# Optimization experiments

Measured on AMD Instinct MI355X. Metric: run time of the kernel, lower is better.

The kernel has to match this reference:

```python
import jax, jax.numpy as jnp
import numpy as np

N = 131072       # total nodes (B graphs x P nodes)
P = 4096         # nodes per graph
B = 32           # graphs in batch
E = 2097152      # edges (avg degree 16)
IN_DIM = 64
HID = 128
OUT = 16
EPS = 1e-5
SLOPE = 0.01


def _degrees(idx):
    # structural degree, clamped to min 1 (as DGL GraphConv does)
    d = jax.ops.segment_sum(jnp.ones((E,), jnp.float32), idx, num_segments=N)
    return jnp.maximum(d, 1.0)


def _graph_conv(x, W, src, dst, ew):
    # DGL GraphConv, norm='both', bias=False, with scalar edge weights:
    # h = D_out^{-1/2} x ; m_v = sum_{(u->v)} w_e h_u ; out = (D_in^{-1/2} m) W
    h = x * jax.lax.rsqrt(_degrees(src))[:, None]
    m = jax.ops.segment_sum(ew[:, None] * h[src], dst, num_segments=N)  # [N, F]
    return (m * jax.lax.rsqrt(_degrees(dst))[:, None]) @ W


def _graph_norm(x, gamma, beta, alpha):
    # GraphNorm (Cai et al. / PyG, batch=None): stats over all nodes per feature
    mu = jnp.mean(x, axis=0)
    c = x - alpha * mu
    var = jnp.mean(c * c, axis=0)
    return c * jax.lax.rsqrt(var + EPS) * gamma + beta


def _mean_nodes(h, gid):
    # per-graph mean readout; every graph has exactly P nodes
    return jax.ops.segment_sum(h, gid, num_segments=B) / P


def setup_inputs() -> dict:
    key = jax.random.key(0)
    ks = jax.random.split(key, 8)
    src = jax.random.randint(ks[0], (E,), 0, N, dtype=jnp.int32)
    # keep edges within each 4096-node graph block (batched DGL graph)
    dst = (src // P) * P + jax.random.randint(ks[1], (E,), 0, P, dtype=jnp.int32)
    features = jax.random.normal(ks[2], (N, IN_DIM), jnp.float32)
    edge_weights = jax.random.uniform(ks[3], (E,), jnp.float32)
    # kaiming/xavier-scale init approximations
    W1 = jax.random.normal(ks[4], (IN_DIM, HID), jnp.float32) * np.sqrt(2.0 / IN_DIM)
    W2 = jax.random.normal(ks[5], (HID, HID), jnp.float32) * np.sqrt(2.0 / HID)
    Wc = jax.random.normal(ks[6], (OUT, 2 * HID), jnp.float32) * np.sqrt(1.0 / (2 * HID))
    ones = jnp.ones((HID,), jnp.float32)
    zeros = jnp.zeros((HID,), jnp.float32)
    return {
        'features': features, 'edge_weights': edge_weights, 'src': src, 'dst': dst,
        'W1': W1, 'W2': W2, 'Wc': Wc,
        'gamma1': ones, 'beta1': zeros, 'alpha1': ones,
        'gamma2': ones, 'beta2': zeros, 'alpha2': ones,
    }


def reference(features, edge_weights, src, dst, W1, W2, Wc,
              gamma1, beta1, alpha1, gamma2, beta2, alpha2):
    gid = jnp.arange(N, dtype=jnp.int32) // P  # node -> graph id
    h1 = _graph_conv(features, W1, src, dst, edge_weights)
    h1 = jax.nn.leaky_relu(_graph_norm(h1, gamma1, beta1, alpha1), SLOPE)
    r1 = _mean_nodes(h1, gid)                  # [B, HID]
    h2 = _graph_conv(h1, W2, src, dst, edge_weights)
    h2 = jax.nn.leaky_relu(_graph_norm(h2, gamma2, beta2, alpha2), SLOPE)
    r2 = _mean_nodes(h2, gid)                  # [B, HID]
    readouts = jnp.concatenate([r1, r2], axis=1)  # [B, 2*HID]
    return readouts @ Wc.T                     # [B, OUT]
```

## Files before the change

kernel.cpp:

```cpp
#include <hip/hip_runtime.h>
#include <hip/hip_fp16.h>

constexpr int NN   = 131072;
constexpr int PP   = 4096;
constexpr int BG   = 32;
constexpr int EE   = 2097152;
constexpr int IND  = 64;
constexpr int HH   = 128;
constexpr int CAP  = 81920;
constexpr float EPSV   = 1e-5f;
constexpr float SLOPEV = 0.01f;

typedef short bf16x8 __attribute__((ext_vector_type(8)));
typedef float f32x4  __attribute__((ext_vector_type(4)));
typedef float f32x2  __attribute__((ext_vector_type(2)));
typedef unsigned u32x4 __attribute__((ext_vector_type(4)));

__device__ __forceinline__ unsigned f2bf(float f) {
    unsigned u = __float_as_uint(f);
    return (u + 0x7FFFu + ((u >> 16) & 1u)) >> 16;
}
__device__ __forceinline__ unsigned pack2bf(float lo, float hi) {
    return f2bf(lo) | (f2bf(hi) << 16);
}
__device__ __forceinline__ float bflo(unsigned p) { return __uint_as_float(p << 16); }
__device__ __forceinline__ float bfhi(unsigned p) { return __uint_as_float(p & 0xFFFF0000u); }
__device__ __forceinline__ float w16(unsigned r) {
    return __half2float(__ushort_as_half((unsigned short)(r >> 16)));
}

template <int K>
__device__ __forceinline__ void packw_body(const float* __restrict__ W,
                                           unsigned short* __restrict__ pw, int t) {
    if (t >= K * 16) return;
    int lane = t & 63, nt = (t >> 6) & 7, kt = t >> 9;
    int kbase = kt * 32 + ((lane >> 4) & 3) * 8;
    int col   = nt * 16 + (lane & 15);
    for (int j = 0; j < 8; j++)
        pw[t * 8 + j] = (unsigned short)f2bf(W[(kbase + j) * HH + col]);
}

__global__ __launch_bounds__(256) void k_prep(const float* __restrict__ features,
                                              unsigned* __restrict__ f8x,
                                              const float* __restrict__ W1,
                                              unsigned short* __restrict__ pw1,
                                              const float* __restrict__ W2,
                                              unsigned short* __restrict__ pw2,
                                              int* __restrict__ gcur,
                                              float* __restrict__ racc,
                                              unsigned* __restrict__ csr2) {
    int b = blockIdx.x, t = threadIdx.x;
    if (b < 8192) {
        int i = b * 256 + t;
        float4 v = ((const float4*)features)[i];
        int w0 = __builtin_amdgcn_cvt_pk_fp8_f32(v.x, v.y, 0, false);
        int w1 = __builtin_amdgcn_cvt_pk_fp8_f32(v.z, v.w, w0, true);
        f8x[i] = (unsigned)w1;
        return;
    }
    if (b == 8192) {
        if (t < BG) gcur[t * 16] = t * CAP;
        for (int i = t; i < 2 * BG * HH; i += 256) racc[i] = 0.f;
        return;
    }
    if (b < 8197) { packw_body<64>(W1, pw1, (b - 8193) * 256 + t); return; }
    if (b < 8205) { packw_body<128>(W2, pw2, (b - 8197) * 256 + t); return; }
    ((uint4*)csr2)[(b - 8205) * 256 + t] = make_uint4(0, 0, 0, 0);
}

__global__ __launch_bounds__(256) void k_part(const int* __restrict__ src,
                                              const int* __restrict__ dst,
                                              const float* __restrict__ ew,
                                              int* __restrict__ gcur,
                                              uint2* __restrict__ recs) {
    __shared__ int cnt[32];
    __shared__ int start[32];
    __shared__ int gbase[32];
    __shared__ uint2 stage[4096];
    int t = threadIdx.x;
    int ebase = blockIdx.x * 4096;
    if (t < 32) cnt[t] = 0;
    __syncthreads();
    int es[16]; int ed[16]; float ev[16];
#pragma unroll
    for (int k = 0; k < 16; k++) {
        int e = ebase + k * 256 + t;
        es[k] = src[e]; ed[k] = dst[e]; ev[k] = ew[e];
        atomicAdd(&cnt[es[k] >> 12], 1);
    }
    __syncthreads();
    if (t == 0) {
        int run = 0;
        for (int g = 0; g < 32; g++) { start[g] = run; run += cnt[g]; }
    }
    __syncthreads();
    if (t < 32) {
        gbase[t] = atomicAdd(&gcur[t * 16], cnt[t]);
        cnt[t] = start[t];
    }
    __syncthreads();
#pragma unroll
    for (int k = 0; k < 16; k++) {
        int g = es[k] >> 12;
        int pos = atomicAdd(&cnt[g], 1);
        stage[pos] = make_uint2((unsigned)(es[k] & 4095) | ((unsigned)(ed[k] & 4095) << 12) |
                                ((unsigned)g << 24), __float_as_uint(ev[k]));
    }
    __syncthreads();
    for (int i = t; i < 4096; i += 256) {
        uint2 r = stage[i];
        int g = r.x >> 24;
        recs[gbase[g] + (i - start[g])] = r;
    }
}

__global__ __launch_bounds__(1024) void k_hist(const uint2* __restrict__ recs,
                                               const int* __restrict__ gcur,
                                               int* __restrict__ shist,
                                               int* __restrict__ dhist) {
    __shared__ int hs[4096];
    __shared__ int hd[4096];
    int t = threadIdx.x;
    int g = blockIdx.x >> 3, c = blockIdx.x & 7;
    int n = gcur[g * 16] - g * CAP;
    int lo = (n * c) >> 3, hi = (n * (c + 1)) >> 3;
    ((int4*)hs)[t] = make_int4(0, 0, 0, 0);
    ((int4*)hd)[t] = make_int4(0, 0, 0, 0);
    __syncthreads();
    const uint2* base = recs + (size_t)g * CAP;
    for (int i = lo + t; i < hi; i += 1024) {
        unsigned x = base[i].x;
        atomicAdd(&hs[x & 4095], 1);
        atomicAdd(&hd[(x >> 12) & 4095], 1);
    }
    __syncthreads();
    ((int4*)(shist + (size_t)blockIdx.x * 4096))[t] = ((int4*)hs)[t];
    ((int4*)(dhist + (size_t)blockIdx.x * 4096))[t] = ((int4*)hd)[t];
}

__global__ __launch_bounds__(1024) void k_offs(int* __restrict__ shist,
                                               int* __restrict__ dhist,
                                               float* __restrict__ rs_s,
                                               float* __restrict__ rsd,
                                               int* __restrict__ degd,
                                               int* __restrict__ offs) {
    __shared__ int partial[1024];
    int t = threadIdx.x, g = blockIdx.x;
    int sdeg[4] = {0, 0, 0, 0}, ddeg[4] = {0, 0, 0, 0};
#pragma unroll
    for (int c = 0; c < 8; c++) {
        int4 sv = ((const int4*)(shist + (size_t)(g * 8 + c) * 4096))[t];
        int4 dv = ((const int4*)(dhist + (size_t)(g * 8 + c) * 4096))[t];
        sdeg[0] += sv.x; sdeg[1] += sv.y; sdeg[2] += sv.z; sdeg[3] += sv.w;
        ddeg[0] += dv.x; ddeg[1] += dv.y; ddeg[2] += dv.z; ddeg[3] += dv.w;
    }
    int pdeg[4];
#pragma unroll
    for (int j = 0; j < 4; j++) {
        int idx = t * 4 + j;
        int vs = sdeg[j]; if (vs < 1) vs = 1;
        rs_s[g * PP + idx] = rsqrtf((float)vs);
        int vd = ddeg[j]; if (vd < 1) vd = 1;
        rsd[g * PP + idx]  = rsqrtf((float)vd);
        pdeg[j] = (ddeg[j] + 3) & ~3;
        degd[g * PP + idx] = pdeg[j];
    }
    partial[t] = pdeg[0] + pdeg[1] + pdeg[2] + pdeg[3];
    __syncthreads();
    for (int off = 1; off < 1024; off <<= 1) {
        int v = partial[t];
        int add = (t >= off) ? partial[t - off] : 0;
        __syncthreads();
        partial[t] = v + add;
        __syncthreads();
    }
    int run = (t == 0) ? 0 : partial[t - 1];
#pragma unroll
    for (int j = 0; j < 4; j++) {
        int idx = t * 4 + j;
        offs[g * PP + idx] = g * CAP + run;
        int nb = run;
        for (int c = 0; c < 8; c++) {
            size_t hidx = (size_t)(g * 8 + c) * 4096 + idx;
            int v = dhist[hidx];
            dhist[hidx] = nb;
            nb += v;
        }
        run += pdeg[j];
    }
}

__global__ __launch_bounds__(1024) void k_place(const uint2* __restrict__ recs,
                                                const int* __restrict__ gcur,
                                                const int* __restrict__ dhist,
                                                const float* __restrict__ rs_s,
                                                unsigned* __restrict__ csr2) {
    __shared__ int cur[4096];
    __shared__ float rss[4096];
    int t = threadIdx.x;
    int g = blockIdx.x >> 3, c = blockIdx.x & 7;
    int n = gcur[g * 16] - g * CAP;
    int lo = (n * c) >> 3, hi = (n * (c + 1)) >> 3;
    ((int4*)cur)[t] = ((const int4*)(dhist + (size_t)blockIdx.x * 4096))[t];
    ((float4*)rss)[t] = ((const float4*)(rs_s + (size_t)g * PP))[t];
    __syncthreads();
    const uint2* base = recs + (size_t)g * CAP;
    unsigned* cbase = csr2 + (size_t)g * CAP;
    for (int i = lo + t; i < hi; i += 1024) {
        uint2 r = base[i];
        int sl = r.x & 4095, dl = (r.x >> 12) & 4095;
        int pos = atomicAdd(&cur[dl], 1);
        float wf = __uint_as_float(r.y) * rss[sl];
        cbase[pos] = (unsigned)sl | ((unsigned)__half_as_ushort(__float2half(wf)) << 16);
    }
}

__device__ __forceinline__ void eacc8(unsigned rec, unsigned q, f32x2& P01, f32x2& P23) {
    f32x2 lo = __builtin_amdgcn_cvt_pk_f32_fp8((int)q, false);
    f32x2 hi = __builtin_amdgcn_cvt_pk_f32_fp8((int)q, true);
    float w = w16(rec);
    P01 += lo * w;
    P23 += hi * w;
}

template <int ROWW>
__device__ __forceinline__ void gath8(const unsigned* __restrict__ hp, u32x4 r,
                                      unsigned& d0, unsigned& d1, unsigned& d2, unsigned& d3) {
    d0 = hp[(r[0] & 4095u) * ROWW];
    d1 = hp[(r[1] & 4095u) * ROWW];
    d2 = hp[(r[2] & 4095u) * ROWW];
    d3 = hp[(r[3] & 4095u) * ROWW];
}

__device__ __forceinline__ void macc8(u32x4 r, unsigned q0, unsigned q1, unsigned q2, unsigned q3,
                                      f32x2& P01, f32x2& P23) {
    eacc8(r[0], q0, P01, P23); eacc8(r[1], q1, P01, P23);
    eacc8(r[2], q2, P01, P23); eacc8(r[3], q3, P01, P23);
}

template <int ROWW>
__device__ __forceinline__ void agg_dual8(const unsigned* __restrict__ hp,
                                          const u32x4* __restrict__ cs4,
                                          int oa, int ca, int ob, int cb,
                                          f32x2& A01, f32x2& A23, f32x2& B01, f32x2& B23) {
    f32x2 z = {0.f, 0.f};
    A01 = z; A23 = z; B01 = z; B23 = z;
    unsigned a4 = ((unsigned)oa) >> 2, b4 = ((unsigned)ob) >> 2;
    int c0 = ca < cb ? ca : cb;
    int cm = ca < cb ? cb : ca;
    int nq = c0 >> 2;
    if (nq > 0) {
        u32x4 ra0 = __builtin_nontemporal_load(cs4 + a4);
        u32x4 rb0 = __builtin_nontemporal_load(cs4 + b4);
        u32x4 ra1 = __builtin_nontemporal_load(cs4 + a4 + 1);
        u32x4 rb1 = __builtin_nontemporal_load(cs4 + b4 + 1);
        unsigned A0, A1, A2, A3, B0, B1, B2, B3;
        unsigned C0, C1, C2, C3, D0, D1, D2, D3;
        gath8<ROWW>(hp, ra0, A0, A1, A2, A3);
        gath8<ROWW>(hp, rb0, B0, B1, B2, B3);
        int k = 0;
        for (; k + 2 <= nq; k += 2) {
            gath8<ROWW>(hp, ra1, C0, C1, C2, C3);
            gath8<ROWW>(hp, rb1, D0, D1, D2, D3);
            u32x4 ra2 = __builtin_nontemporal_load(cs4 + a4 + k + 2);
            u32x4 rb2 = __builtin_nontemporal_load(cs4 + b4 + k + 2);
            macc8(ra0, A0, A1, A2, A3, A01, A23);
            macc8(rb0, B0, B1, B2, B3, B01, B23);
            gath8<ROWW>(hp, ra2, A0, A1, A2, A3);
            gath8<ROWW>(hp, rb2, B0, B1, B2, B3);
            u32x4 ra3 = __builtin_nontemporal_load(cs4 + a4 + k + 3);
            u32x4 rb3 = __builtin_nontemporal_load(cs4 + b4 + k + 3);
            macc8(ra1, C0, C1, C2, C3, A01, A23);
            macc8(rb1, D0, D1, D2, D3, B01, B23);
            ra0 = ra2; rb0 = rb2; ra1 = ra3; rb1 = rb3;
        }
        if (k < nq) {
            macc8(ra0, A0, A1, A2, A3, A01, A23);
            macc8(rb0, B0, B1, B2, B3, B01, B23);
        }
    }
    if (cm > c0) {
        bool an = ca > cb;
        unsigned t4 = an ? a4 : b4;
        int kq1 = cm >> 2, nq0 = c0 >> 2;
        f32x2 E01 = z, E23 = z;
        u32x4 rr = __builtin_nontemporal_load(cs4 + t4 + nq0);
        for (int k = nq0; k < kq1; k++) {
            unsigned q0, q1, q2, q3;
            gath8<ROWW>(hp, rr, q0, q1, q2, q3);
            u32x4 nr = __builtin_nontemporal_load(cs4 + t4 + k + 1);
            macc8(rr, q0, q1, q2, q3, E01, E23);
            rr = nr;
        }
        if (an) { A01 += E01; A23 += E23; }
        else    { B01 += E01; B23 += E23; }
    }
}

__global__ __launch_bounds__(256) void k_aggemm1(const unsigned* __restrict__ f8x,
                                                 const unsigned* __restrict__ csr2,
                                                 const int* __restrict__ offs,
                                                 const int* __restrict__ degd,
                                                 const float* __restrict__ rsd,
                                                 const short* __restrict__ PW,
                                                 unsigned short* __restrict__ C,
                                                 float* __restrict__ part) {
    constexpr int WP = 36;
    __shared__ unsigned lds[64 * WP];
    __shared__ float s1[HH], s2[HH];
    int t = threadIdx.x;
    if (t < HH) { s1[t] = 0.f; s2[t] = 0.f; }
    int bid = blockIdx.x;
    int xcd = bid & 7, idx = bid >> 3;
    int g = xcd * 4 + (idx >> 6);
    int node0 = g * PP + (idx & 63) * 64;
    int lane = t & 63, wv = t >> 6;
    int q = lane >> 4, ql = lane & 15;
    const unsigned* hp8 = f8x + (size_t)((unsigned)(g * PP)) * 16 + ql;
    const u32x4* cs4 = (const u32x4*)csr2;
#pragma unroll
    for (int p = 0; p < 2; p++) {
        int lrA = wv * 16 + p * 8 + q * 2;
        int va = node0 + lrA;
        int2 oo = *(const int2*)(offs + va);
        int2 dd = *(const int2*)(degd + va);
        f32x2 A01, A23, B01, B23;
        agg_dual8<16>(hp8, cs4, oo.x, dd.x, oo.y, dd.y, A01, A23, B01, B23);
        float2 rr2 = *(const float2*)(rsd + va);
        *(uint2*)&lds[lrA * WP + ql * 2] =
            make_uint2(pack2bf(A01.x * rr2.x, A01.y * rr2.x),
                       pack2bf(A23.x * rr2.x, A23.y * rr2.x));
        *(uint2*)&lds[(lrA + 1) * WP + ql * 2] =
            make_uint2(pack2bf(B01.x * rr2.y, B01.y * rr2.y),
                       pack2bf(B23.x * rr2.y, B23.y * rr2.y));
    }
    __syncthreads();
    int m = lane & 15, quad = lane >> 4;
    bf16x8 a[2];
#pragma unroll
    for (int kt = 0; kt < 2; kt++)
        a[kt] = *(const bf16x8*)&lds[(wv * 16 + m) * WP + kt * 16 + quad * 4];
#pragma unroll
    for (int nt = 0; nt < 8; nt++) {
        f32x4 acc = {0.f, 0.f, 0.f, 0.f};
#pragma unroll
        for (int kt = 0; kt < 2; kt++) {
            bf16x8 b = *(const bf16x8*)(PW + ((size_t)(kt * 8 + nt) * 64 + lane) * 8);
            acc = __builtin_amdgcn_mfma_f32_16x16x32_bf16(a[kt], b, acc, 0, 0, 0);
        }
        int col = nt * 16 + m;
        int r0 = node0 + wv * 16 + quad * 4;
        float ps = 0.f, pq = 0.f;
#pragma unroll
        for (int r = 0; r < 4; r++) {
            C[(size_t)(r0 + r) * HH + col] = (unsigned short)f2bf(acc[r]);
            ps += acc[r]; pq += acc[r] * acc[r];
        }
        atomicAdd(&s1[col], ps);
        atomicAdd(&s2[col], pq);
    }
    __syncthreads();
    if (t < HH) {
        part[bid * 256 + t]      = s1[t];
        part[bid * 256 + HH + t] = s2[t];
    }
}

__global__ __launch_bounds__(256) void k_aggemm2(const unsigned* __restrict__ f8,
                                                 const unsigned* __restrict__ csr2,
                                                 const int* __restrict__ offs,
                                                 const int* __restrict__ degd,
                                                 const float* __restrict__ rsd,
                                                 const short* __restrict__ PW,
                                                 unsigned short* __restrict__ C,
                                                 float* __restrict__ part) {
    constexpr int WP = 68;
    __shared__ unsigned lds[64 * WP];
    __shared__ float s1[HH], s2[HH];
    int t = threadIdx.x;
    if (t < HH) { s1[t] = 0.f; s2[t] = 0.f; }
    int bid = blockIdx.x;
    int xcd = bid & 7, idx = bid >> 3;
    int g = xcd * 4 + (idx >> 6);
    int node0 = g * PP + (idx & 63) * 64;
    int lane = t & 63, wv = t >> 6;
    int half = lane >> 5, sl = lane & 31;
    const unsigned* hp8 = f8 + (size_t)((unsigned)(g * PP)) * 32 + sl;
    const u32x4* cs4 = (const u32x4*)csr2;
#pragma unroll
    for (int p = 0; p < 4; p++) {
        int lrA = wv * 16 + p * 4 + half * 2;
        int va = node0 + lrA;
        int2 oo = *(const int2*)(offs + va);
        int2 dd = *(const int2*)(degd + va);
        f32x2 A01, A23, B01, B23;
        agg_dual8<32>(hp8, cs4, oo.x, dd.x, oo.y, dd.y, A01, A23, B01, B23);
        float2 rr2 = *(const float2*)(rsd + va);
        *(uint2*)&lds[lrA * WP + sl * 2] =
            make_uint2(pack2bf(A01.x * rr2.x, A01.y * rr2.x),
                       pack2bf(A23.x * rr2.x, A23.y * rr2.x));
        *(uint2*)&lds[(lrA + 1) * WP + sl * 2] =
            make_uint2(pack2bf(B01.x * rr2.y, B01.y * rr2.y),
                       pack2bf(B23.x * rr2.y, B23.y * rr2.y));
    }
    __syncthreads();
    int m = lane & 15, quad = lane >> 4;
    bf16x8 a[4];
#pragma unroll
    for (int kt = 0; kt < 4; kt++)
        a[kt] = *(const bf16x8*)&lds[(wv * 16 + m) * WP + kt * 16 + quad * 4];
#pragma unroll
    for (int nt = 0; nt < 8; nt++) {
        f32x4 acc = {0.f, 0.f, 0.f, 0.f};
#pragma unroll
        for (int kt = 0; kt < 4; kt++) {
            bf16x8 b = *(const bf16x8*)(PW + ((size_t)(kt * 8 + nt) * 64 + lane) * 8);
            acc = __builtin_amdgcn_mfma_f32_16x16x32_bf16(a[kt], b, acc, 0, 0, 0);
        }
        int col = nt * 16 + m;
        int r0 = node0 + wv * 16 + quad * 4;
        float ps = 0.f, pq = 0.f;
#pragma unroll
        for (int r = 0; r < 4; r++) {
            C[(size_t)(r0 + r) * HH + col] = (unsigned short)f2bf(acc[r]);
            ps += acc[r]; pq += acc[r] * acc[r];
        }
        atomicAdd(&s1[col], ps);
        atomicAdd(&s2[col], pq);
    }
    __syncthreads();
    if (t < HH) {
        part[bid * 256 + t]      = s1[t];
        part[bid * 256 + HH + t] = s2[t];
    }
}

__global__ __launch_bounds__(256) void k_red(const float* __restrict__ part,
                                             float* __restrict__ pb) {
    int t = threadIdx.x, b = blockIdx.x;
    float s = 0.f;
    for (int r = 0; r < 32; r++) s += part[(size_t)(b * 32 + r) * 256 + t];
    pb[b * 256 + t] = s;
}

__global__ void k_coef(const float* __restrict__ pb, const float* __restrict__ gamma,
                       const float* __restrict__ beta, const float* __restrict__ alpha,
                       float* __restrict__ ab) {
    int t = threadIdx.x;
    float s = 0.f;
    for (int b = 0; b < 64; b++) s += pb[b * 256 + t];
    __shared__ float sh[256];
    sh[t] = s;
    __syncthreads();
    if (t < 128) {
        float mu = sh[t] * (1.f / NN);
        float e2 = sh[128 + t] * (1.f / NN);
        float al = alpha[t];
        float var = e2 - (2.f * al - al * al) * mu * mu;
        float a = rsqrtf(var + EPSV) * gamma[t];
        ab[t] = a;
        ab[HH + t] = beta[t] - al * mu * a;
    }
}

template <bool WRITE>
__global__ __launch_bounds__(256) void k_normro(const unsigned* __restrict__ h,
                                                const float* __restrict__ ab,
                                                float* __restrict__ racc,
                                                unsigned short* __restrict__ f8) {
    int fp = threadIdx.x & 63;
    int q  = threadIdx.x >> 6;
    int node0 = blockIdx.x * 64;
    int g = node0 / PP;
    float a0 = ab[2 * fp], a1 = ab[2 * fp + 1];
    float b0 = ab[HH + 2 * fp], b1 = ab[HH + 2 * fp + 1];
    float s0 = 0.f, s1 = 0.f;
    for (int i = q; i < 64; i += 4) {
        size_t idx = (size_t)(node0 + i) * 64 + fp;
        unsigned v = h[idx];
        float x0 = fmaf(a0, bflo(v), b0); x0 = x0 > 0.f ? x0 : SLOPEV * x0;
        float x1 = fmaf(a1, bfhi(v), b1); x1 = x1 > 0.f ? x1 : SLOPEV * x1;
        if (WRITE) f8[idx] = (unsigned short)__builtin_amdgcn_cvt_pk_fp8_f32(x0, x1, 0, false);
        s0 += x0; s1 += x1;
    }
    __shared__ float sh[512];
    sh[threadIdx.x] = s0;
    sh[256 + threadIdx.x] = s1;
    __syncthreads();
    if (q == 0) {
        float t0 = s0 + sh[64 + fp] + sh[128 + fp] + sh[192 + fp];
        float t1 = s1 + sh[256 + 64 + fp] + sh[256 + 128 + fp] + sh[256 + 192 + fp];
        atomicAdd(&racc[g * HH + 2 * fp],     t0);
        atomicAdd(&racc[g * HH + 2 * fp + 1], t1);
    }
}

__global__ void k_final(const float* __restrict__ racc1, const float* __restrict__ racc2,
                        const float* __restrict__ Wc, float* __restrict__ out) {
    int t = threadIdx.x;
    int b = t >> 4, o = t & 15;
    float acc = 0.f;
    for (int f = 0; f < HH; f++) acc += racc1[b * HH + f] * Wc[o * (2 * HH) + f];
    for (int f = 0; f < HH; f++) acc += racc2[b * HH + f] * Wc[o * (2 * HH) + HH + f];
    out[t] = acc * (1.f / PP);
}

extern "C" void kernel_launch(void* const* d_in, const int* in_sizes, int n_in,
                              void* d_out, int out_size, void* d_ws, size_t ws_size,
                              hipStream_t stream) {
    const float* features = (const float*)d_in[0];
    const float* ew       = (const float*)d_in[1];
    const int*   src      = (const int*)d_in[2];
    const int*   dst      = (const int*)d_in[3];
    const float* W1       = (const float*)d_in[4];
    const float* W2       = (const float*)d_in[5];
    const float* Wc       = (const float*)d_in[6];
    const float* gamma1   = (const float*)d_in[7];
    const float* beta1    = (const float*)d_in[8];
    const float* alpha1   = (const float*)d_in[9];
    const float* gamma2   = (const float*)d_in[10];
    const float* beta2    = (const float*)d_in[11];
    const float* alpha2   = (const float*)d_in[12];
    float* out = (float*)d_out;

    char* w = (char*)d_ws;
    int*    gcur   = (int*)(w + 0);
    float*  racc1  = (float*)(w + (16u << 10));
    float*  racc2  = (float*)(w + (32u << 10));
    float*  ab1    = (float*)(w + (48u << 10));
    float*  ab2    = (float*)(w + (52u << 10));
    unsigned short* pw1 = (unsigned short*)(w + (64u << 10));
    unsigned short* pw2 = (unsigned short*)(w + (80u << 10));
    float*  pb     = (float*)(w + (128u << 10));
    float*  rs_s   = (float*)(w + (1024u << 10));
    float*  rsd    = (float*)(w + (1536u << 10));
    int*    degd   = (int*)(w + (2048u << 10));
    int*    offs   = (int*)(w + (2560u << 10));
    float*  part   = (float*)(w + (3u << 20));
    int*    shist  = (int*)(w + (5u << 20));
    int*    dhist  = (int*)(w + (9u << 20));
    unsigned* csr2 = (unsigned*)(w + (13u << 20));
    unsigned* mbuf = (unsigned*)(w + (23u << 20));
    unsigned* hbuf = (unsigned*)(w + (55u << 20));
    uint2*    recs = (uint2*)(w + (87u << 20));
    unsigned* f8x  = (unsigned*)(w + (107u << 20));
    unsigned* f8buf= (unsigned*)(w + (123u << 20));

    k_prep<<<10765, 256, 0, stream>>>(features, f8x, W1, pw1, W2, pw2, gcur, racc1, csr2);

    k_part<<<EE / 4096, 256, 0, stream>>>(src, dst, ew, gcur, recs);
    k_hist<<<BG * 8, 1024, 0, stream>>>(recs, gcur, shist, dhist);
    k_offs<<<BG, 1024, 0, stream>>>(shist, dhist, rs_s, rsd, degd, offs);
    k_place<<<BG * 8, 1024, 0, stream>>>(recs, gcur, dhist, rs_s, csr2);

    k_aggemm1<<<NN / 64, 256, 0, stream>>>(f8x, csr2, offs, degd, rsd,
                                           (const short*)pw1, (unsigned short*)hbuf, part);
    k_red<<<64, 256, 0, stream>>>(part, pb);
    k_coef<<<1, 256, 0, stream>>>(pb, gamma1, beta1, alpha1, ab1);
    k_normro<true><<<NN / 64, 256, 0, stream>>>(hbuf, ab1, racc1, (unsigned short*)f8buf);

    k_aggemm2<<<NN / 64, 256, 0, stream>>>(f8buf, csr2, offs, degd, rsd,
                                           (const short*)pw2, (unsigned short*)mbuf, part);
    k_red<<<64, 256, 0, stream>>>(part, pb);
    k_coef<<<1, 256, 0, stream>>>(pb, gamma2, beta2, alpha2, ab2);
    k_normro<false><<<NN / 64, 256, 0, stream>>>(mbuf, ab2, racc2, nullptr);

    k_final<<<1, 512, 0, stream>>>(racc1, racc2, Wc, out);
}
```

Before: 370.7 us.

## Widen per-lane gather to 8 fp8 features and drop software pipelining

The edge aggregation now has each lane gather 8 bytes (8 fp8 features) per neighbor instead of 4. Fewer lanes cover a node row, so each wavefront processes more node pairs at once: layer 1 drops from two passes to one, and layer 2 from four passes to two. The explicit double-buffered prefetch of CSR records with nontemporal loads is replaced by a simple loop of plain loads. This halves the number of gather instructions and increases memory-level parallelism per wave, but it loses the manual prefetch overlap and raises register pressure.

```diff
diff --git a/kernel.cpp b/kernel.cpp
--- a/kernel.cpp
+++ b/kernel.cpp
@@ -14,7 +14,6 @@
 typedef short bf16x8 __attribute__((ext_vector_type(8)));
 typedef float f32x4  __attribute__((ext_vector_type(4)));
 typedef float f32x2  __attribute__((ext_vector_type(2)));
-typedef unsigned u32x4 __attribute__((ext_vector_type(4)));
 
 __device__ __forceinline__ unsigned f2bf(float f) {
     unsigned u = __float_as_uint(f);
@@ -215,85 +214,64 @@
     }
 }
 
-__device__ __forceinline__ void eacc8(unsigned rec, unsigned q, f32x2& P01, f32x2& P23) {
-    f32x2 lo = __builtin_amdgcn_cvt_pk_f32_fp8((int)q, false);
-    f32x2 hi = __builtin_amdgcn_cvt_pk_f32_fp8((int)q, true);
+__device__ __forceinline__ void eacc2(unsigned rec, uint2 q,
+                                      f32x2& P01, f32x2& P23, f32x2& P45, f32x2& P67) {
+    f32x2 l0 = __builtin_amdgcn_cvt_pk_f32_fp8((int)q.x, false);
+    f32x2 h0 = __builtin_amdgcn_cvt_pk_f32_fp8((int)q.x, true);
+    f32x2 l1 = __builtin_amdgcn_cvt_pk_f32_fp8((int)q.y, false);
+    f32x2 h1 = __builtin_amdgcn_cvt_pk_f32_fp8((int)q.y, true);
     float w = w16(rec);
-    P01 += lo * w;
-    P23 += hi * w;
-}
-
-template <int ROWW>
-__device__ __forceinline__ void gath8(const unsigned* __restrict__ hp, u32x4 r,
-                                      unsigned& d0, unsigned& d1, unsigned& d2, unsigned& d3) {
-    d0 = hp[(r[0] & 4095u) * ROWW];
-    d1 = hp[(r[1] & 4095u) * ROWW];
-    d2 = hp[(r[2] & 4095u) * ROWW];
-    d3 = hp[(r[3] & 4095u) * ROWW];
-}
-
-__device__ __forceinline__ void macc8(u32x4 r, unsigned q0, unsigned q1, unsigned q2, unsigned q3,
-                                      f32x2& P01, f32x2& P23) {
-    eacc8(r[0], q0, P01, P23); eacc8(r[1], q1, P01, P23);
-    eacc8(r[2], q2, P01, P23); eacc8(r[3], q3, P01, P23);
-}
-
-template <int ROWW>
-__device__ __forceinline__ void agg_dual8(const unsigned* __restrict__ hp,
-                                          const u32x4* __restrict__ cs4,
-                                          int oa, int ca, int ob, int cb,
-                                          f32x2& A01, f32x2& A23, f32x2& B01, f32x2& B23) {
+    P01 += l0 * w; P23 += h0 * w; P45 += l1 * w; P67 += h1 * w;
+}
+
+template <int RW2>
+__device__ __forceinline__ void agg_dual_w(const uint2* __restrict__ hp,
+                                           const unsigned* __restrict__ csr2,
+                                           int oa, int ca, int ob, int cb,
+                                           f32x2& A01, f32x2& A23, f32x2& A45, f32x2& A67,
+                                           f32x2& B01, f32x2& B23, f32x2& B45, f32x2& B67) {
     f32x2 z = {0.f, 0.f};
-    A01 = z; A23 = z; B01 = z; B23 = z;
-    unsigned a4 = ((unsigned)oa) >> 2, b4 = ((unsigned)ob) >> 2;
+    A01 = z; A23 = z; A45 = z; A67 = z;
+    B01 = z; B23 = z; B45 = z; B67 = z;
     int c0 = ca < cb ? ca : cb;
     int cm = ca < cb ? cb : ca;
-    int nq = c0 >> 2;
-    if (nq > 0) {
-        u32x4 ra0 = __builtin_nontemporal_load(cs4 + a4);
-        u32x4 rb0 = __builtin_nontemporal_load(cs4 + b4);
-        u32x4 ra1 = __builtin_nontemporal_load(cs4 + a4 + 1);
-        u32x4 rb1 = __builtin_nontemporal_load(cs4 + b4 + 1);
-        unsigned A0, A1, A2, A3, B0, B1, B2, B3;
-        unsigned C0, C1, C2, C3, D0, D1, D2, D3;
-        gath8<ROWW>(hp, ra0, A0, A1, A2, A3);
-        gath8<ROWW>(hp, rb0, B0, B1, B2, B3);
-        int k = 0;
-        for (; k + 2 <= nq; k += 2) {
-            gath8<ROWW>(hp, ra1, C0, C1, C2, C3);
-            gath8<ROWW>(hp, rb1, D0, D1, D2, D3);
-            u32x4 ra2 = __builtin_nontemporal_load(cs4 + a4 + k + 2);
-            u32x4 rb2 = __builtin_nontemporal_load(cs4 + b4 + k + 2);
-            macc8(ra0, A0, A1, A2, A3, A01, A23);
-            macc8(rb0, B0, B1, B2, B3, B01, B23);
-            gath8<ROWW>(hp, ra2, A0, A1, A2, A3);
-            gath8<ROWW>(hp, rb2, B0, B1, B2, B3);
-            u32x4 ra3 = __builtin_nontemporal_load(cs4 + a4 + k + 3);
-            u32x4 rb3 = __builtin_nontemporal_load(cs4 + b4 + k + 3);
-            macc8(ra1, C0, C1, C2, C3, A01, A23);
-            macc8(rb1, D0, D1, D2, D3, B01, B23);
-            ra0 = ra2; rb0 = rb2; ra1 = ra3; rb1 = rb3;
+    int i = 0;
+    for (; i < c0; i += 4) {
+        uint4 ra = *(const uint4*)(csr2 + oa + i);
+        uint4 rb = *(const uint4*)(csr2 + ob + i);
+        uint2 qa0 = hp[(ra.x & 4095u) * RW2];
+        uint2 qa1 = hp[(ra.y & 4095u) * RW2];
+        uint2 qa2 = hp[(ra.z & 4095u) * RW2];
+        uint2 qa3 = hp[(ra.w & 4095u) * RW2];
+        uint2 qb0 = hp[(rb.x & 4095u) * RW2];
+        uint2 qb1 = hp[(rb.y & 4095u) * RW2];
+        uint2 qb2 = hp[(rb.z & 4095u) * RW2];
+        uint2 qb3 = hp[(rb.w & 4095u) * RW2];
+        eacc2(ra.x, qa0, A01, A23, A45, A67);
+        eacc2(ra.y, qa1, A01, A23, A45, A67);
+        eacc2(ra.z, qa2, A01, A23, A45, A67);
+        eacc2(ra.w, qa3, A01, A23, A45, A67);
+        eacc2(rb.x, qb0, B01, B23, B45, B67);
+        eacc2(rb.y, qb1, B01, B23, B45, B67);
+        eacc2(rb.z, qb2, B01, B23, B45, B67);
+        eacc2(rb.w, qb3, B01, B23, B45, B67);
+    }
+    if (i < cm) {
+        int ot = (ca > cb) ? oa : ob;
+        f32x2 E01 = z, E23 = z, E45 = z, E67 = z;
+        for (; i < cm; i += 4) {
+            uint4 rr = *(const uint4*)(csr2 + ot + i);
+            uint2 q0 = hp[(rr.x & 4095u) * RW2];
+            uint2 q1 = hp[(rr.y & 4095u) * RW2];
+            uint2 q2 = hp[(rr.z & 4095u) * RW2];
+            uint2 q3 = hp[(rr.w & 4095u) * RW2];
+            eacc2(rr.x, q0, E01, E23, E45, E67);
+            eacc2(rr.y, q1, E01, E23, E45, E67);
+            eacc2(rr.z, q2, E01, E23, E45, E67);
+            eacc2(rr.w, q3, E01, E23, E45, E67);
         }
-        if (k < nq) {
-            macc8(ra0, A0, A1, A2, A3, A01, A23);
-            macc8(rb0, B0, B1, B2, B3, B01, B23);
-        }
-    }
-    if (cm > c0) {
-        bool an = ca > cb;
-        unsigned t4 = an ? a4 : b4;
-        int kq1 = cm >> 2, nq0 = c0 >> 2;
-        f32x2 E01 = z, E23 = z;
-        u32x4 rr = __builtin_nontemporal_load(cs4 + t4 + nq0);
-        for (int k = nq0; k < kq1; k++) {
-            unsigned q0, q1, q2, q3;
-            gath8<ROWW>(hp, rr, q0, q1, q2, q3);
-            u32x4 nr = __builtin_nontemporal_load(cs4 + t4 + k + 1);
-            macc8(rr, q0, q1, q2, q3, E01, E23);
-            rr = nr;
-        }
-        if (an) { A01 += E01; A23 += E23; }
-        else    { B01 += E01; B23 += E23; }
+        if (ca > cb) { A01 += E01; A23 += E23; A45 += E45; A67 += E67; }
+        else         { B01 += E01; B23 += E23; B45 += E45; B67 += E67; }
     }
 }
 
@@ -315,24 +293,23 @@
     int g = xcd * 4 + (idx >> 6);
     int node0 = g * PP + (idx & 63) * 64;
     int lane = t & 63, wv = t >> 6;
-    int q = lane >> 4, ql = lane & 15;
-    const unsigned* hp8 = f8x + (size_t)((unsigned)(g * PP)) * 16 + ql;
-    const u32x4* cs4 = (const u32x4*)csr2;
-#pragma unroll
-    for (int p = 0; p < 2; p++) {
-        int lrA = wv * 16 + p * 8 + q * 2;
+    int grp = lane >> 3, gl = lane & 7;
+    const uint2* hp = (const uint2*)f8x + (size_t)((unsigned)(g * PP)) * 8 + gl;
+    {
+        int lrA = wv * 16 + grp * 2;
         int va = node0 + lrA;
         int2 oo = *(const int2*)(offs + va);
         int2 dd = *(const int2*)(degd + va);
-        f32x2 A01, A23, B01, B23;
-        agg_dual8<16>(hp8, cs4, oo.x, dd.x, oo.y, dd.y, A01, A23, B01, B23);
+        f32x2 A01, A23, A45, A67, B01, B23, B45, B67;
+        agg_dual_w<8>(hp, csr2, oo.x, dd.x, oo.y, dd.y,
+                      A01, A23, A45, A67, B01, B23, B45, B67);
         float2 rr2 = *(const float2*)(rsd + va);
-        *(uint2*)&lds[lrA * WP + ql * 2] =
-            make_uint2(pack2bf(A01.x * rr2.x, A01.y * rr2.x),
-                       pack2bf(A23.x * rr2.x, A23.y * rr2.x));
-        *(uint2*)&lds[(lrA + 1) * WP + ql * 2] =
-            make_uint2(pack2bf(B01.x * rr2.y, B01.y * rr2.y),
-                       pack2bf(B23.x * rr2.y, B23.y * rr2.y));
+        *(uint4*)&lds[lrA * WP + gl * 4] = make_uint4(
+            pack2bf(A01.x * rr2.x, A01.y * rr2.x), pack2bf(A23.x * rr2.x, A23.y * rr2.x),
+            pack2bf(A45.x * rr2.x, A45.y * rr2.x), pack2bf(A67.x * rr2.x, A67.y * rr2.x));
+        *(uint4*)&lds[(lrA + 1) * WP + gl * 4] = make_uint4(
+            pack2bf(B01.x * rr2.y, B01.y * rr2.y), pack2bf(B23.x * rr2.y, B23.y * rr2.y),
+            pack2bf(B45.x * rr2.y, B45.y * rr2.y), pack2bf(B67.x * rr2.y, B67.y * rr2.y));
     }
     __syncthreads();
     int m = lane & 15, quad = lane >> 4;
@@ -384,24 +361,23 @@
     int g = xcd * 4 + (idx >> 6);
     int node0 = g * PP + (idx & 63) * 64;
     int lane = t & 63, wv = t >> 6;
-    int half = lane >> 5, sl = lane & 31;
-    const unsigned* hp8 = f8 + (size_t)((unsigned)(g * PP)) * 32 + sl;
-    const u32x4* cs4 = (const u32x4*)csr2;
-#pragma unroll
-    for (int p = 0; p < 4; p++) {
-        int lrA = wv * 16 + p * 4 + half * 2;
+    int grp = lane >> 4, gl = lane & 15;
+    const uint2* hp = (const uint2*)f8 + (size_t)((unsigned)(g * PP)) * 16 + gl;
+    for (int p = 0; p < 2; p++) {
+        int lrA = wv * 16 + p * 8 + grp * 2;
         int va = node0 + lrA;
         int2 oo = *(const int2*)(offs + va);
         int2 dd = *(const int2*)(degd + va);
-        f32x2 A01, A23, B01, B23;
-        agg_dual8<32>(hp8, cs4, oo.x, dd.x, oo.y, dd.y, A01, A23, B01, B23);
+        f32x2 A01, A23, A45, A67, B01, B23, B45, B67;
+        agg_dual_w<16>(hp, csr2, oo.x, dd.x, oo.y, dd.y,
+                       A01, A23, A45, A67, B01, B23, B45, B67);
         float2 rr2 = *(const float2*)(rsd + va);
-        *(uint2*)&lds[lrA * WP + sl * 2] =
-            make_uint2(pack2bf(A01.x * rr2.x, A01.y * rr2.x),
-                       pack2bf(A23.x * rr2.x, A23.y * rr2.x));
-        *(uint2*)&lds[(lrA + 1) * WP + sl * 2] =
-            make_uint2(pack2bf(B01.x * rr2.y, B01.y * rr2.y),
-                       pack2bf(B23.x * rr2.y, B23.y * rr2.y));
+        *(uint4*)&lds[lrA * WP + gl * 4] = make_uint4(
+            pack2bf(A01.x * rr2.x, A01.y * rr2.x), pack2bf(A23.x * rr2.x, A23.y * rr2.x),
+            pack2bf(A45.x * rr2.x, A45.y * rr2.x), pack2bf(A67.x * rr2.x, A67.y * rr2.x));
+        *(uint4*)&lds[(lrA + 1) * WP + gl * 4] = make_uint4(
+            pack2bf(B01.x * rr2.y, B01.y * rr2.y), pack2bf(B23.x * rr2.y, B23.y * rr2.y),
+            pack2bf(B45.x * rr2.y, B45.y * rr2.y), pack2bf(B67.x * rr2.y, B67.y * rr2.y));
     }
     __syncthreads();
     int m = lane & 15, quad = lane >> 4;
```

Measured after the change: 358.9 us. -3.2%, faster.
